# Kernel optimization log

Measured on AMD Instinct MI355X. Metric: run time of the kernel, lower is better.

Reference implementation:

```python
import jax, jax.numpy as jnp
import numpy as np

D = 1  # dilation


def _unfold3x3(x, d):
    # x: [B, C, H, W] -> [B, H*W, 9, C]; matches torch.nn.Unfold(kernel_size=3,
    # dilation=d, padding=d, stride=1) followed by the module's reshapes.
    B, C, H, W = x.shape
    xp = jnp.pad(x, ((0, 0), (0, 0), (d, d), (d, d)))
    pats = [xp[:, :, i * d:i * d + H, j * d:j * d + W] for i in range(3) for j in range(3)]
    p = jnp.stack(pats, axis=0)  # [9, B, C, H, W], kernel positions row-major (center = 4)
    return p.transpose(1, 3, 4, 0, 2).reshape(B, H * W, 9, C)


def _masked_bn(h, m, gamma, beta, eps=1e-5):
    # BatchNorm1d in training mode applied only to rows selected by bool mask m
    # (the torch code gathers rows, BNs them, scatters back into zeros).
    # Stats are the biased mean/var over the selected rows, per channel.
    axes = tuple(range(h.ndim - 1))
    mf = m[..., None].astype(h.dtype)
    n = jnp.maximum(mf.sum(), 1.0)
    mean = (h * mf).sum(axes) / n
    var = (((h - mean) ** 2 * mf)).sum(axes) / n
    return (h - mean) * jax.lax.rsqrt(var + eps) * gamma + beta


def setup_inputs() -> dict:
    key = jax.random.key(0)
    ks = jax.random.split(key, 8)
    B, H, W = 2, 64, 1024
    Cin, Cout, Cm = 64, 64, 4
    s = 0.1
    x = jax.random.normal(ks[0], (B, Cm + Cin, H, W), jnp.float32)
    mask = (jax.random.uniform(ks[1], (B, 1, H, W)) > 0.3).astype(jnp.float32)
    return {
        "x": x,
        "mask": mask,
        "w1": jax.random.normal(ks[2], (8, Cm), jnp.float32) * s,
        "bn1_g": jnp.ones(8, jnp.float32),
        "bn1_b": jnp.zeros(8, jnp.float32),
        "w2": jax.random.normal(ks[3], (1, 8), jnp.float32) * s,
        "b2": jnp.zeros(1, jnp.float32),
        "g1": jax.random.normal(ks[4], (8, Cm), jnp.float32) * s,
        "gbn1_g": jnp.ones(8, jnp.float32),
        "gbn1_b": jnp.zeros(8, jnp.float32),
        "g2": jax.random.normal(ks[5], (8, 8), jnp.float32) * s,
        "gbn2_g": jnp.ones(8, jnp.float32),
        "gbn2_b": jnp.zeros(8, jnp.float32),
        "w_agg": jax.random.normal(ks[6], (Cout, 72 + Cin), jnp.float32) * s,
        "abn_g": jnp.ones(Cout, jnp.float32),
        "abn_b": jnp.zeros(Cout, jnp.float32),
    }


def reference(x, mask, w1, bn1_g, bn1_b, w2, b2, g1, gbn1_g, gbn1_b, g2, gbn2_g, gbn2_b, w_agg, abn_g, abn_b):
    B, C, H, W = x.shape
    xu = _unfold3x3(x, D)                      # [B, HW, 9, C]
    mu = _unfold3x3(mask, D)[..., 0]           # [B, HW, 9]
    msel = mu > 0                              # valid-neighbor mask
    mp0 = msel[:, :, 4]                        # valid-center mask [B, HW]
    pn = xu[..., :4] - xu[:, :, 4:5, :4]       # relative meta coords [B, HW, 9, 4]
    feats = xu[..., 4:]                        # neighbor features [B, HW, 9, Cin]

    # weight branch (dense compute + mask == torch's gather/scatter)
    h = _masked_bn(pn @ w1.T, msel, bn1_g, bn1_b)
    h = jax.nn.relu(h) @ w2.T + b2             # [B, HW, 9, 1]
    wts = jnp.where(msel, h[..., 0], 0.0)      # zeros at invalid neighbors pre-softmax
    wts = jax.nn.softmax(wts, axis=-1)[..., None]

    fagg = (wts * feats).sum(axis=2)           # [B, HW, Cin]

    # geo branch
    g = jax.nn.relu(_masked_bn(pn @ g1.T, msel, gbn1_g, gbn1_b))
    g = jax.nn.relu(_masked_bn(g @ g2.T, msel, gbn2_g, gbn2_b))
    g = jnp.where(msel[..., None], g, 0.0)
    g = (wts * g).reshape(B, H * W, 72)

    # aggregation over valid centers
    out = jnp.concatenate([fagg, g], axis=-1) @ w_agg.T
    out = jax.nn.relu(_masked_bn(out, mp0, abn_g, abn_b))
    out = jnp.where(mp0[..., None], out, 0.0)  # [B, HW, Cout]
    return out.transpose(0, 2, 1).reshape(B, -1, H, W)  # fold with k=1 == reshape
```

## Files before the change

### kernel.cpp

```cpp
#include <hip/hip_runtime.h>

#define HW_ 65536
#define W_ 1024
#define H_ 64
#define B_ 2
#define C_ 68
#define NPIX 131072
#define EPS 1e-5f

typedef __attribute__((ext_vector_type(8))) short short8;
typedef __attribute__((ext_vector_type(4))) float floatx4;

__device__ __forceinline__ unsigned short f2bf(float f) {
  unsigned u = __float_as_uint(f);
  u += 0x7fffu + ((u >> 16) & 1u);
  return (unsigned short)(u >> 16);
}
__device__ __forceinline__ unsigned pack2(float a, float b) {
  return (unsigned)f2bf(a) | ((unsigned)f2bf(b) << 16);
}
__device__ __forceinline__ float wred(float v) {
  v += __shfl_xor(v, 1);  v += __shfl_xor(v, 2);  v += __shfl_xor(v, 4);
  v += __shfl_xor(v, 8);  v += __shfl_xor(v, 16); v += __shfl_xor(v, 32);
  return v;
}
__device__ __forceinline__ int swz_tile(int bid) {
  return (bid & 7) * 64 + (bid >> 3);
}

__global__ __launch_bounds__(256) void k_stats1(
    const float* __restrict__ x, const float* __restrict__ mask,
    const float* __restrict__ w1, const float* __restrict__ g1,
    float* __restrict__ ws) {
  float acc[34];
#pragma unroll
  for (int i = 0; i < 34; i++) acc[i] = 0.f;

  int p = swz_tile(blockIdx.x) * 256 + threadIdx.x;
  {
    int b = p >> 16, s = p & (HW_ - 1);
    int h = s >> 10, w = s & (W_ - 1);
    const float* xb = x + (size_t)b * C_ * HW_;
    const float* mb = mask + (size_t)b * HW_;
    float xc0 = xb[s], xc1 = xb[HW_ + s], xc2 = xb[2 * HW_ + s], xc3 = xb[3 * HW_ + s];
    acc[33] += (mb[s] > 0.f) ? 1.f : 0.f;
#pragma unroll
    for (int k = 0; k < 9; k++) {
      int di = k / 3 - 1, dj = k % 3 - 1;
      int hh = h + di, ww = w + dj;
      bool inb = ((unsigned)hh < (unsigned)H_) && ((unsigned)ww < (unsigned)W_);
      int ns = hh * W_ + ww;
      float mval = inb ? mb[ns] : 0.f;
      if (mval > 0.f) {
        float pn0 = xb[ns] - xc0;
        float pn1 = xb[HW_ + ns] - xc1;
        float pn2 = xb[2 * HW_ + ns] - xc2;
        float pn3 = xb[3 * HW_ + ns] - xc3;
        acc[32] += 1.f;
#pragma unroll
        for (int o = 0; o < 8; o++) {
          float ta = pn0 * w1[o * 4] + pn1 * w1[o * 4 + 1] + pn2 * w1[o * 4 + 2] + pn3 * w1[o * 4 + 3];
          acc[o] += ta; acc[8 + o] += ta * ta;
          float tg = pn0 * g1[o * 4] + pn1 * g1[o * 4 + 1] + pn2 * g1[o * 4 + 2] + pn3 * g1[o * 4 + 3];
          acc[16 + o] += tg; acc[24 + o] += tg * tg;
        }
      }
    }
  }
  __shared__ float red[4][34];
  int lane = threadIdx.x & 63, wave = threadIdx.x >> 6;
#pragma unroll
  for (int i = 0; i < 34; i++) {
    float r = wred(acc[i]);
    if (lane == 0) red[wave][i] = r;
  }
  __syncthreads();
  if (threadIdx.x < 34)
    atomicAdd(&ws[threadIdx.x],
              red[0][threadIdx.x] + red[1][threadIdx.x] + red[2][threadIdx.x] + red[3][threadIdx.x]);
}

__global__ __launch_bounds__(256) void k_stats2(
    const float* __restrict__ x, const float* __restrict__ mask,
    const float* __restrict__ g1, const float* __restrict__ gbn1_g,
    const float* __restrict__ gbn1_b, const float* __restrict__ g2,
    float* __restrict__ ws) {
  __shared__ float sc[8], sh[8];
  if (threadIdx.x < 8) {
    int o = threadIdx.x;
    float n = fmaxf(ws[32], 1.f);
    float mean = ws[16 + o] / n;
    float var = ws[24 + o] / n - mean * mean;
    float s = gbn1_g[o] * rsqrtf(var + EPS);
    sc[o] = s; sh[o] = gbn1_b[o] - mean * s;
  }
  __syncthreads();

  float acc[16];
#pragma unroll
  for (int i = 0; i < 16; i++) acc[i] = 0.f;

  int p = swz_tile(blockIdx.x) * 256 + threadIdx.x;
  {
    int b = p >> 16, s = p & (HW_ - 1);
    int h = s >> 10, w = s & (W_ - 1);
    const float* xb = x + (size_t)b * C_ * HW_;
    const float* mb = mask + (size_t)b * HW_;
    float xc0 = xb[s], xc1 = xb[HW_ + s], xc2 = xb[2 * HW_ + s], xc3 = xb[3 * HW_ + s];
#pragma unroll
    for (int k = 0; k < 9; k++) {
      int di = k / 3 - 1, dj = k % 3 - 1;
      int hh = h + di, ww = w + dj;
      bool inb = ((unsigned)hh < (unsigned)H_) && ((unsigned)ww < (unsigned)W_);
      int ns = hh * W_ + ww;
      float mval = inb ? mb[ns] : 0.f;
      if (mval > 0.f) {
        float pn0 = xb[ns] - xc0;
        float pn1 = xb[HW_ + ns] - xc1;
        float pn2 = xb[2 * HW_ + ns] - xc2;
        float pn3 = xb[3 * HW_ + ns] - xc3;
        float gb[8];
#pragma unroll
        for (int o = 0; o < 8; o++) {
          float tg = pn0 * g1[o * 4] + pn1 * g1[o * 4 + 1] + pn2 * g1[o * 4 + 2] + pn3 * g1[o * 4 + 3];
          gb[o] = fmaxf(sc[o] * tg + sh[o], 0.f);
        }
#pragma unroll
        for (int j = 0; j < 8; j++) {
          float t2 = 0.f;
#pragma unroll
          for (int o = 0; o < 8; o++) t2 += gb[o] * g2[j * 8 + o];
          acc[j] += t2; acc[8 + j] += t2 * t2;
        }
      }
    }
  }
  __shared__ float red[4][16];
  int lane = threadIdx.x & 63, wave = threadIdx.x >> 6;
#pragma unroll
  for (int i = 0; i < 16; i++) {
    float r = wred(acc[i]);
    if (lane == 0) red[wave][i] = r;
  }
  __syncthreads();
  if (threadIdx.x < 16)
    atomicAdd(&ws[40 + threadIdx.x],
              red[0][threadIdx.x] + red[1][threadIdx.x] + red[2][threadIdx.x] + red[3][threadIdx.x]);
}

__global__ __launch_bounds__(256) void k_fused(
    const float* __restrict__ x, const float* __restrict__ mask,
    const float* __restrict__ w1, const float* __restrict__ bn1_g,
    const float* __restrict__ bn1_b, const float* __restrict__ w2,
    const float* __restrict__ b2, const float* __restrict__ g1,
    const float* __restrict__ gbn1_g, const float* __restrict__ gbn1_b,
    const float* __restrict__ g2, const float* __restrict__ gbn2_g,
    const float* __restrict__ gbn2_b, const float* __restrict__ w_agg,
    const float* __restrict__ ws, float* __restrict__ out_pre,
    float* __restrict__ wsum) {
  __shared__ uint4 vecA[17][256];
  __shared__ float sA[8], hA[8], sG1[8], hG1[8], sG2[8], hG2[8];

  if (threadIdx.x < 24) {
    int o = threadIdx.x & 7;
    float n = fmaxf(ws[32], 1.f);
    float sum, sum2, gma, bta;
    if (threadIdx.x < 8)       { sum = ws[o];      sum2 = ws[8 + o];  gma = bn1_g[o];  bta = bn1_b[o]; }
    else if (threadIdx.x < 16) { sum = ws[16 + o]; sum2 = ws[24 + o]; gma = gbn1_g[o]; bta = gbn1_b[o]; }
    else                       { sum = ws[40 + o]; sum2 = ws[48 + o]; gma = gbn2_g[o]; bta = gbn2_b[o]; }
    float mean = sum / n, var = sum2 / n - mean * mean;
    float s = gma * rsqrtf(var + EPS);
    float sft = bta - mean * s;
    if (threadIdx.x < 8)       { sA[o] = s;  hA[o] = sft; }
    else if (threadIdx.x < 16) { sG1[o] = s; hG1[o] = sft; }
    else                       { sG2[o] = s; hG2[o] = sft; }
  }
  __syncthreads();

  int tile = swz_tile(blockIdx.x);
  int p0 = tile * 256;
  int p = p0 + threadIdx.x;
  int b = p >> 16, s = p & (HW_ - 1);
  int h = s >> 10, w = s & (W_ - 1);
  const float* xb = x + (size_t)b * C_ * HW_;
  const float* mb = mask + (size_t)b * HW_;
  float xc0 = xb[s], xc1 = xb[HW_ + s], xc2 = xb[2 * HW_ + s], xc3 = xb[3 * HW_ + s];
  float b2v = b2[0];

  float ev[9]; int nsv[9]; bool inbv[9], mselv[9];
  float mx = -1e30f;
#pragma unroll
  for (int k = 0; k < 9; k++) {
    int di = k / 3 - 1, dj = k % 3 - 1;
    int hh = h + di, ww = w + dj;
    bool inb = ((unsigned)hh < (unsigned)H_) && ((unsigned)ww < (unsigned)W_);
    int ns = hh * W_ + ww;
    inbv[k] = inb; nsv[k] = ns;
    float mval = inb ? mb[ns] : 0.f;
    bool msel = mval > 0.f;
    mselv[k] = msel;
    float wp = 0.f;
    if (msel) {
      float pn0 = xb[ns] - xc0;
      float pn1 = xb[HW_ + ns] - xc1;
      float pn2 = xb[2 * HW_ + ns] - xc2;
      float pn3 = xb[3 * HW_ + ns] - xc3;
      float accw = 0.f;
#pragma unroll
      for (int o = 0; o < 8; o++) {
        float ta = pn0 * w1[o * 4] + pn1 * w1[o * 4 + 1] + pn2 * w1[o * 4 + 2] + pn3 * w1[o * 4 + 3];
        accw += fmaxf(sA[o] * ta + hA[o], 0.f) * w2[o];
      }
      wp = accw + b2v;
    }
    ev[k] = wp;
    mx = fmaxf(mx, wp);
  }
  float den = 0.f;
#pragma unroll
  for (int k = 0; k < 9; k++) { ev[k] = __expf(ev[k] - mx); den += ev[k]; }
  float inv = 1.f / den;

  float fagg[64];
#pragma unroll
  for (int c = 0; c < 64; c++) fagg[c] = 0.f;

#pragma unroll
  for (int k = 0; k < 9; k++) {
    float wt = ev[k] * inv;
    int ns = nsv[k];
    uint4 pk; pk.x = pk.y = pk.z = pk.w = 0u;
    if (mselv[k]) {
      float pn0 = xb[ns] - xc0;
      float pn1 = xb[HW_ + ns] - xc1;
      float pn2 = xb[2 * HW_ + ns] - xc2;
      float pn3 = xb[3 * HW_ + ns] - xc3;
      float gb[8];
#pragma unroll
      for (int o = 0; o < 8; o++) {
        float tg = pn0 * g1[o * 4] + pn1 * g1[o * 4 + 1] + pn2 * g1[o * 4 + 2] + pn3 * g1[o * 4 + 3];
        gb[o] = fmaxf(sG1[o] * tg + hG1[o], 0.f);
      }
      float gv[8];
#pragma unroll
      for (int j = 0; j < 8; j++) {
        float t2 = 0.f;
#pragma unroll
        for (int o = 0; o < 8; o++) t2 += gb[o] * g2[j * 8 + o];
        float gg = fmaxf(sG2[j] * t2 + hG2[j], 0.f);
        gv[j] = wt * gg;
      }
      pk.x = pack2(gv[0], gv[1]); pk.y = pack2(gv[2], gv[3]);
      pk.z = pack2(gv[4], gv[5]); pk.w = pack2(gv[6], gv[7]);
    }
    vecA[8 + k][threadIdx.x] = pk;
    if (inbv[k]) {
      const float* xf = xb + 4 * HW_ + ns;
#pragma unroll
      for (int c = 0; c < 64; c++) fagg[c] += wt * xf[c * HW_];
    }
  }
#pragma unroll
  for (int c = 0; c < 64; c += 8) {
    uint4 pk;
    pk.x = pack2(fagg[c], fagg[c + 1]);     pk.y = pack2(fagg[c + 2], fagg[c + 3]);
    pk.z = pack2(fagg[c + 4], fagg[c + 5]); pk.w = pack2(fagg[c + 6], fagg[c + 7]);
    vecA[c >> 3][threadIdx.x] = pk;
  }
  __syncthreads();

  int lane = threadIdx.x & 63, wave = threadIdx.x >> 6;
  int q = lane >> 4, r = lane & 15;

  short8 Bf[4][5];
#pragma unroll
  for (int nt = 0; nt < 4; nt++) {
    int n = nt * 16 + r;
#pragma unroll
    for (int ks = 0; ks < 5; ks++) {
      int k0 = ks * 32 + q * 8;
      uint4 pk; pk.x = pk.y = pk.z = pk.w = 0u;
      if (k0 < 136) {
        float4 f0 = *reinterpret_cast<const float4*>(w_agg + n * 136 + k0);
        float4 f1 = *reinterpret_cast<const float4*>(w_agg + n * 136 + k0 + 4);
        pk.x = pack2(f0.x, f0.y); pk.y = pack2(f0.z, f0.w);
        pk.z = pack2(f1.x, f1.y); pk.w = pack2(f1.z, f1.w);
      }
      Bf[nt][ks] = *reinterpret_cast<short8*>(&pk);
    }
  }

  floatx4 acc[4][4];
#pragma unroll
  for (int m = 0; m < 4; m++)
#pragma unroll
    for (int nt = 0; nt < 4; nt++) acc[m][nt] = (floatx4){0.f, 0.f, 0.f, 0.f};

#pragma unroll
  for (int m = 0; m < 4; m++) {
    int mt = wave * 4 + m;
    int pix = mt * 16 + r;
    short8 Af[5];
#pragma unroll
    for (int ks = 0; ks < 5; ks++) {
      int chunk = ks * 4 + q;
      if (chunk < 17)
        Af[ks] = *reinterpret_cast<const short8*>(&vecA[chunk][pix]);
      else
        Af[ks] = (short8){0, 0, 0, 0, 0, 0, 0, 0};
    }
#pragma unroll
    for (int nt = 0; nt < 4; nt++)
#pragma unroll
      for (int ks = 0; ks < 5; ks++)
        acc[m][nt] = __builtin_amdgcn_mfma_f32_16x16x32_bf16(Af[ks], Bf[nt][ks], acc[m][nt], 0, 0, 0);
  }

  float aS[4] = {0.f, 0.f, 0.f, 0.f}, aQ[4] = {0.f, 0.f, 0.f, 0.f};
  int s0 = p0 & (HW_ - 1);
#pragma unroll
  for (int m = 0; m < 4; m++) {
    int mt = wave * 4 + m;
    int srow = s0 + mt * 16 + q * 4;
    float4 mv = *reinterpret_cast<const float4*>(mb + srow);
    float m0 = (mv.x > 0.f) ? 1.f : 0.f, m1 = (mv.y > 0.f) ? 1.f : 0.f;
    float m2 = (mv.z > 0.f) ? 1.f : 0.f, m3 = (mv.w > 0.f) ? 1.f : 0.f;
#pragma unroll
    for (int nt = 0; nt < 4; nt++) {
      int ch = nt * 16 + r;
      float4 ov;
      ov.x = acc[m][nt][0]; ov.y = acc[m][nt][1];
      ov.z = acc[m][nt][2]; ov.w = acc[m][nt][3];
      aS[nt] += ov.x * m0 + ov.y * m1 + ov.z * m2 + ov.w * m3;
      aQ[nt] += ov.x * ov.x * m0 + ov.y * ov.y * m1 + ov.z * ov.z * m2 + ov.w * ov.w * m3;
      *reinterpret_cast<float4*>(out_pre + ((size_t)(b * 64 + ch)) * HW_ + srow) = ov;
    }
  }

  __syncthreads();
  float* rS = (float*)&vecA[0][0];
  float* rQ = rS + 256;
#pragma unroll
  for (int nt = 0; nt < 4; nt++) {
    float v1 = aS[nt], v2 = aQ[nt];
    v1 += __shfl_xor(v1, 16); v1 += __shfl_xor(v1, 32);
    v2 += __shfl_xor(v2, 16); v2 += __shfl_xor(v2, 32);
    if (lane < 16) { rS[wave * 64 + nt * 16 + lane] = v1; rQ[wave * 64 + nt * 16 + lane] = v2; }
  }
  __syncthreads();
  if (threadIdx.x < 64) {
    atomicAdd(&wsum[64 + threadIdx.x],
              rS[threadIdx.x] + rS[64 + threadIdx.x] + rS[128 + threadIdx.x] + rS[192 + threadIdx.x]);
    atomicAdd(&wsum[128 + threadIdx.x],
              rQ[threadIdx.x] + rQ[64 + threadIdx.x] + rQ[128 + threadIdx.x] + rQ[192 + threadIdx.x]);
  }
}

__global__ __launch_bounds__(256) void k_final(
    const float* __restrict__ out_pre, const float* __restrict__ mask,
    const float* __restrict__ abn_g, const float* __restrict__ abn_b,
    const float* __restrict__ ws, float* __restrict__ out) {
  __shared__ float sc[64], sh[64];
  if (threadIdx.x < 64) {
    int c = threadIdx.x;
    float n0 = fmaxf(ws[33], 1.f);
    float mean = ws[64 + c] / n0;
    float var = ws[128 + c] / n0 - mean * mean;
    float s = abn_g[c] * rsqrtf(var + EPS);
    sc[c] = s; sh[c] = abn_b[c] - mean * s;
  }
  __syncthreads();
  int i4 = (blockIdx.x * 256 + threadIdx.x) * 4;
  if (i4 >= B_ * 64 * HW_) return;
  int c = (i4 >> 16) & 63;
  int b = i4 >> 22;
  int s = i4 & (HW_ - 1);
  float4 v = *reinterpret_cast<const float4*>(out_pre + i4);
  float4 m = *reinterpret_cast<const float4*>(mask + (size_t)b * HW_ + s);
  float4 o;
  o.x = (m.x > 0.f) ? fmaxf(v.x * sc[c] + sh[c], 0.f) : 0.f;
  o.y = (m.y > 0.f) ? fmaxf(v.y * sc[c] + sh[c], 0.f) : 0.f;
  o.z = (m.z > 0.f) ? fmaxf(v.z * sc[c] + sh[c], 0.f) : 0.f;
  o.w = (m.w > 0.f) ? fmaxf(v.w * sc[c] + sh[c], 0.f) : 0.f;
  *reinterpret_cast<float4*>(out + i4) = o;
}

extern "C" void kernel_launch(void* const* d_in, const int* in_sizes, int n_in,
                              void* d_out, int out_size, void* d_ws, size_t ws_size,
                              hipStream_t stream) {
  const float* x      = (const float*)d_in[0];
  const float* mask   = (const float*)d_in[1];
  const float* w1     = (const float*)d_in[2];
  const float* bn1_g  = (const float*)d_in[3];
  const float* bn1_b  = (const float*)d_in[4];
  const float* w2     = (const float*)d_in[5];
  const float* b2     = (const float*)d_in[6];
  const float* g1     = (const float*)d_in[7];
  const float* gbn1_g = (const float*)d_in[8];
  const float* gbn1_b = (const float*)d_in[9];
  const float* g2     = (const float*)d_in[10];
  const float* gbn2_g = (const float*)d_in[11];
  const float* gbn2_b = (const float*)d_in[12];
  const float* w_agg  = (const float*)d_in[13];
  const float* abn_g  = (const float*)d_in[14];
  const float* abn_b  = (const float*)d_in[15];
  float* out = (float*)d_out;

  size_t need = 1024 + (size_t)NPIX * 64 * 4;
  if (ws_size < need) return;

  float* wsf = (float*)d_ws;
  float* out_pre = (float*)((char*)d_ws + 1024);

  hipMemsetAsync(d_ws, 0, 1024, stream);
  k_stats1<<<512, 256, 0, stream>>>(x, mask, w1, g1, wsf);
  k_stats2<<<512, 256, 0, stream>>>(x, mask, g1, gbn1_g, gbn1_b, g2, wsf);
  k_fused<<<512, 256, 0, stream>>>(x, mask, w1, bn1_g, bn1_b, w2, b2, g1,
                                   gbn1_g, gbn1_b, g2, gbn2_g, gbn2_b, w_agg,
                                   wsf, out_pre, wsf);
  k_final<<<8192, 256, 0, stream>>>(out_pre, mask, abn_g, abn_b, wsf, out);
}
```

Measured before the change: 222.9 us.

## Use moment stats for BN1, split neighbors across waves, store bf16 intermediate

```diff
diff --git a/kernel.cpp b/kernel.cpp
--- a/kernel.cpp
+++ b/kernel.cpp
@@ -3,10 +3,13 @@
 #define HW_ 65536
 #define W_ 1024
 #define H_ 64
-#define B_ 2
 #define C_ 68
 #define NPIX 131072
 #define EPS 1e-5f
+
+#define ST2OFF 256
+#define ATOFF 512
+#define OUTPRE_BYTE 16384
 
 typedef __attribute__((ext_vector_type(8))) short short8;
 typedef __attribute__((ext_vector_type(4))) float floatx4;
@@ -19,65 +22,60 @@
 __device__ __forceinline__ unsigned pack2(float a, float b) {
   return (unsigned)f2bf(a) | ((unsigned)f2bf(b) << 16);
 }
+__device__ __forceinline__ float bf2f(unsigned short u) {
+  return __uint_as_float(((unsigned)u) << 16);
+}
 __device__ __forceinline__ float wred(float v) {
   v += __shfl_xor(v, 1);  v += __shfl_xor(v, 2);  v += __shfl_xor(v, 4);
   v += __shfl_xor(v, 8);  v += __shfl_xor(v, 16); v += __shfl_xor(v, 32);
   return v;
 }
-__device__ __forceinline__ int swz_tile(int bid) {
-  return (bid & 7) * 64 + (bid >> 3);
-}
 
 __global__ __launch_bounds__(256) void k_stats1(
     const float* __restrict__ x, const float* __restrict__ mask,
-    const float* __restrict__ w1, const float* __restrict__ g1,
     float* __restrict__ ws) {
-  float acc[34];
-#pragma unroll
-  for (int i = 0; i < 34; i++) acc[i] = 0.f;
-
-  int p = swz_tile(blockIdx.x) * 256 + threadIdx.x;
-  {
-    int b = p >> 16, s = p & (HW_ - 1);
-    int h = s >> 10, w = s & (W_ - 1);
-    const float* xb = x + (size_t)b * C_ * HW_;
-    const float* mb = mask + (size_t)b * HW_;
-    float xc0 = xb[s], xc1 = xb[HW_ + s], xc2 = xb[2 * HW_ + s], xc3 = xb[3 * HW_ + s];
-    acc[33] += (mb[s] > 0.f) ? 1.f : 0.f;
-#pragma unroll
-    for (int k = 0; k < 9; k++) {
-      int di = k / 3 - 1, dj = k % 3 - 1;
-      int hh = h + di, ww = w + dj;
-      bool inb = ((unsigned)hh < (unsigned)H_) && ((unsigned)ww < (unsigned)W_);
-      int ns = hh * W_ + ww;
-      float mval = inb ? mb[ns] : 0.f;
-      if (mval > 0.f) {
-        float pn0 = xb[ns] - xc0;
-        float pn1 = xb[HW_ + ns] - xc1;
-        float pn2 = xb[2 * HW_ + ns] - xc2;
-        float pn3 = xb[3 * HW_ + ns] - xc3;
-        acc[32] += 1.f;
-#pragma unroll
-        for (int o = 0; o < 8; o++) {
-          float ta = pn0 * w1[o * 4] + pn1 * w1[o * 4 + 1] + pn2 * w1[o * 4 + 2] + pn3 * w1[o * 4 + 3];
-          acc[o] += ta; acc[8 + o] += ta * ta;
-          float tg = pn0 * g1[o * 4] + pn1 * g1[o * 4 + 1] + pn2 * g1[o * 4 + 2] + pn3 * g1[o * 4 + 3];
-          acc[16 + o] += tg; acc[24 + o] += tg * tg;
-        }
-      }
-    }
-  }
-  __shared__ float red[4][34];
-  int lane = threadIdx.x & 63, wave = threadIdx.x >> 6;
-#pragma unroll
-  for (int i = 0; i < 34; i++) {
+  __shared__ float red[4][16];
+  const int tid = threadIdx.x, bid = blockIdx.x;
+  const int lane = tid & 63, wave = tid >> 6;
+  const int seg = (bid & 7) * 256 + (bid >> 3);
+  const int sg = seg * 64 + lane;
+  const int b = sg >> 16, s = sg & (HW_ - 1);
+  const int h = s >> 10, w = s & (W_ - 1);
+  const float* xb = x + (size_t)b * C_ * HW_;
+  const float* mb = mask + (size_t)b * HW_;
+
+  float acc[16];
+#pragma unroll
+  for (int i = 0; i < 16; i++) acc[i] = 0.f;
+  float xc0 = xb[s], xc1 = xb[HW_ + s], xc2 = xb[2 * HW_ + s], xc3 = xb[3 * HW_ + s];
+  if (wave == 0) acc[15] = (mb[s] > 0.f) ? 1.f : 0.f;
+
+  for (int k = wave; k < 9; k += 4) {
+    int di = k / 3 - 1, dj = k % 3 - 1;
+    int hh = h + di, ww = w + dj;
+    bool inb = ((unsigned)hh < (unsigned)H_) && ((unsigned)ww < (unsigned)W_);
+    int ns = inb ? hh * W_ + ww : s;
+    float mk = (inb && mb[ns] > 0.f) ? 1.f : 0.f;
+    float p0 = xb[ns] - xc0;
+    float p1 = xb[HW_ + ns] - xc1;
+    float p2 = xb[2 * HW_ + ns] - xc2;
+    float p3 = xb[3 * HW_ + ns] - xc3;
+    float q0 = mk * p0, q1 = mk * p1, q2 = mk * p2, q3 = mk * p3;
+    acc[0] += q0; acc[1] += q1; acc[2] += q2; acc[3] += q3;
+    acc[4] += q0 * p0; acc[5] += q0 * p1; acc[6] += q0 * p2; acc[7] += q0 * p3;
+    acc[8] += q1 * p1; acc[9] += q1 * p2; acc[10] += q1 * p3;
+    acc[11] += q2 * p2; acc[12] += q2 * p3;
+    acc[13] += q3 * p3;
+    acc[14] += mk;
+  }
+#pragma unroll
+  for (int i = 0; i < 16; i++) {
     float r = wred(acc[i]);
     if (lane == 0) red[wave][i] = r;
   }
   __syncthreads();
-  if (threadIdx.x < 34)
-    atomicAdd(&ws[threadIdx.x],
-              red[0][threadIdx.x] + red[1][threadIdx.x] + red[2][threadIdx.x] + red[3][threadIdx.x]);
+  if (tid < 16)
+    atomicAdd(&ws[tid * 16], red[0][tid] + red[1][tid] + red[2][tid] + red[3][tid]);
 }
 
 __global__ __launch_bounds__(256) void k_stats2(
@@ -85,67 +83,71 @@
     const float* __restrict__ g1, const float* __restrict__ gbn1_g,
     const float* __restrict__ gbn1_b, const float* __restrict__ g2,
     float* __restrict__ ws) {
-  __shared__ float sc[8], sh[8];
-  if (threadIdx.x < 8) {
-    int o = threadIdx.x;
-    float n = fmaxf(ws[32], 1.f);
-    float mean = ws[16 + o] / n;
-    float var = ws[24 + o] / n - mean * mean;
-    float s = gbn1_g[o] * rsqrtf(var + EPS);
-    sc[o] = s; sh[o] = gbn1_b[o] - mean * s;
-  }
-  __syncthreads();
+  __shared__ float scl[16];
+  __shared__ float red[4][16];
+  const int tid = threadIdx.x, bid = blockIdx.x;
+  const int lane = tid & 63, wave = tid >> 6;
+
+  if (tid < 8) {
+    int o = tid;
+    float n = fmaxf(ws[224], 1.f);
+    const float* wv = g1 + o * 4;
+    float w0 = wv[0], w1v = wv[1], w2v = wv[2], w3v = wv[3];
+    float sum = w0 * ws[0] + w1v * ws[16] + w2v * ws[32] + w3v * ws[48];
+    float quad = w0 * (w0 * ws[64] + 2.f * (w1v * ws[80] + w2v * ws[96] + w3v * ws[112]))
+               + w1v * (w1v * ws[128] + 2.f * (w2v * ws[144] + w3v * ws[160]))
+               + w2v * (w2v * ws[176] + 2.f * w3v * ws[192])
+               + w3v * w3v * ws[208];
+    float mean = sum / n, var = quad / n - mean * mean;
+    float sv = gbn1_g[o] * rsqrtf(var + EPS);
+    scl[o] = sv; scl[8 + o] = gbn1_b[o] - mean * sv;
+  }
+  __syncthreads();
+
+  const int seg = (bid & 7) * 256 + (bid >> 3);
+  const int sg = seg * 64 + lane;
+  const int b = sg >> 16, s = sg & (HW_ - 1);
+  const int h = s >> 10, w = s & (W_ - 1);
+  const float* xb = x + (size_t)b * C_ * HW_;
+  const float* mb = mask + (size_t)b * HW_;
 
   float acc[16];
 #pragma unroll
   for (int i = 0; i < 16; i++) acc[i] = 0.f;
-
-  int p = swz_tile(blockIdx.x) * 256 + threadIdx.x;
-  {
-    int b = p >> 16, s = p & (HW_ - 1);
-    int h = s >> 10, w = s & (W_ - 1);
-    const float* xb = x + (size_t)b * C_ * HW_;
-    const float* mb = mask + (size_t)b * HW_;
-    float xc0 = xb[s], xc1 = xb[HW_ + s], xc2 = xb[2 * HW_ + s], xc3 = xb[3 * HW_ + s];
-#pragma unroll
-    for (int k = 0; k < 9; k++) {
-      int di = k / 3 - 1, dj = k % 3 - 1;
-      int hh = h + di, ww = w + dj;
-      bool inb = ((unsigned)hh < (unsigned)H_) && ((unsigned)ww < (unsigned)W_);
-      int ns = hh * W_ + ww;
-      float mval = inb ? mb[ns] : 0.f;
-      if (mval > 0.f) {
-        float pn0 = xb[ns] - xc0;
-        float pn1 = xb[HW_ + ns] - xc1;
-        float pn2 = xb[2 * HW_ + ns] - xc2;
-        float pn3 = xb[3 * HW_ + ns] - xc3;
-        float gb[8];
-#pragma unroll
-        for (int o = 0; o < 8; o++) {
-          float tg = pn0 * g1[o * 4] + pn1 * g1[o * 4 + 1] + pn2 * g1[o * 4 + 2] + pn3 * g1[o * 4 + 3];
-          gb[o] = fmaxf(sc[o] * tg + sh[o], 0.f);
-        }
-#pragma unroll
-        for (int j = 0; j < 8; j++) {
-          float t2 = 0.f;
-#pragma unroll
-          for (int o = 0; o < 8; o++) t2 += gb[o] * g2[j * 8 + o];
-          acc[j] += t2; acc[8 + j] += t2 * t2;
-        }
-      }
-    }
-  }
-  __shared__ float red[4][16];
-  int lane = threadIdx.x & 63, wave = threadIdx.x >> 6;
+  float xc0 = xb[s], xc1 = xb[HW_ + s], xc2 = xb[2 * HW_ + s], xc3 = xb[3 * HW_ + s];
+
+  for (int k = wave; k < 9; k += 4) {
+    int di = k / 3 - 1, dj = k % 3 - 1;
+    int hh = h + di, ww = w + dj;
+    bool inb = ((unsigned)hh < (unsigned)H_) && ((unsigned)ww < (unsigned)W_);
+    int ns = inb ? hh * W_ + ww : s;
+    float mk = (inb && mb[ns] > 0.f) ? 1.f : 0.f;
+    float pn0 = xb[ns] - xc0;
+    float pn1 = xb[HW_ + ns] - xc1;
+    float pn2 = xb[2 * HW_ + ns] - xc2;
+    float pn3 = xb[3 * HW_ + ns] - xc3;
+    float gb[8];
+#pragma unroll
+    for (int o = 0; o < 8; o++) {
+      float tg = pn0 * g1[o * 4] + pn1 * g1[o * 4 + 1] + pn2 * g1[o * 4 + 2] + pn3 * g1[o * 4 + 3];
+      gb[o] = fmaxf(scl[o] * tg + scl[8 + o], 0.f);
+    }
+#pragma unroll
+    for (int j = 0; j < 8; j++) {
+      float t2 = 0.f;
+#pragma unroll
+      for (int o = 0; o < 8; o++) t2 += gb[o] * g2[j * 8 + o];
+      acc[j] += mk * t2; acc[8 + j] += mk * t2 * t2;
+    }
+  }
 #pragma unroll
   for (int i = 0; i < 16; i++) {
     float r = wred(acc[i]);
     if (lane == 0) red[wave][i] = r;
   }
   __syncthreads();
-  if (threadIdx.x < 16)
-    atomicAdd(&ws[40 + threadIdx.x],
-              red[0][threadIdx.x] + red[1][threadIdx.x] + red[2][threadIdx.x] + red[3][threadIdx.x]);
+  if (tid < 16)
+    atomicAdd(&ws[ST2OFF + tid * 16], red[0][tid] + red[1][tid] + red[2][tid] + red[3][tid]);
 }
 
 __global__ __launch_bounds__(256) void k_fused(
@@ -156,30 +158,41 @@
     const float* __restrict__ gbn1_g, const float* __restrict__ gbn1_b,
     const float* __restrict__ g2, const float* __restrict__ gbn2_g,
     const float* __restrict__ gbn2_b, const float* __restrict__ w_agg,
-    const float* __restrict__ ws, float* __restrict__ out_pre,
-    float* __restrict__ wsum) {
+    float* __restrict__ ws) {
   __shared__ uint4 vecA[17][256];
   __shared__ float sA[8], hA[8], sG1[8], hG1[8], sG2[8], hG2[8];
-
-  if (threadIdx.x < 24) {
-    int o = threadIdx.x & 7;
-    float n = fmaxf(ws[32], 1.f);
-    float sum, sum2, gma, bta;
-    if (threadIdx.x < 8)       { sum = ws[o];      sum2 = ws[8 + o];  gma = bn1_g[o];  bta = bn1_b[o]; }
-    else if (threadIdx.x < 16) { sum = ws[16 + o]; sum2 = ws[24 + o]; gma = gbn1_g[o]; bta = gbn1_b[o]; }
-    else                       { sum = ws[40 + o]; sum2 = ws[48 + o]; gma = gbn2_g[o]; bta = gbn2_b[o]; }
-    float mean = sum / n, var = sum2 / n - mean * mean;
-    float s = gma * rsqrtf(var + EPS);
-    float sft = bta - mean * s;
-    if (threadIdx.x < 8)       { sA[o] = s;  hA[o] = sft; }
-    else if (threadIdx.x < 16) { sG1[o] = s; hG1[o] = sft; }
-    else                       { sG2[o] = s; hG2[o] = sft; }
-  }
-  __syncthreads();
-
-  int tile = swz_tile(blockIdx.x);
+  const int tid = threadIdx.x;
+
+  if (tid < 24) {
+    int o = tid & 7;
+    float n = fmaxf(ws[224], 1.f);
+    float sv, sft;
+    if (tid < 16) {
+      const float* wv = (tid < 8) ? (w1 + o * 4) : (g1 + o * 4);
+      float w0 = wv[0], w1v = wv[1], w2v = wv[2], w3v = wv[3];
+      float sum = w0 * ws[0] + w1v * ws[16] + w2v * ws[32] + w3v * ws[48];
+      float quad = w0 * (w0 * ws[64] + 2.f * (w1v * ws[80] + w2v * ws[96] + w3v * ws[112]))
+                 + w1v * (w1v * ws[128] + 2.f * (w2v * ws[144] + w3v * ws[160]))
+                 + w2v * (w2v * ws[176] + 2.f * w3v * ws[192])
+                 + w3v * w3v * ws[208];
+      float gma = (tid < 8) ? bn1_g[o] : gbn1_g[o];
+      float bta = (tid < 8) ? bn1_b[o] : gbn1_b[o];
+      float mean = sum / n, var = quad / n - mean * mean;
+      sv = gma * rsqrtf(var + EPS); sft = bta - mean * sv;
+    } else {
+      float sum = ws[ST2OFF + o * 16], sum2 = ws[ST2OFF + (8 + o) * 16];
+      float mean = sum / n, var = sum2 / n - mean * mean;
+      sv = gbn2_g[o] * rsqrtf(var + EPS); sft = gbn2_b[o] - mean * sv;
+    }
+    if (tid < 8)       { sA[o] = sv;  hA[o] = sft; }
+    else if (tid < 16) { sG1[o] = sv; hG1[o] = sft; }
+    else               { sG2[o] = sv; hG2[o] = sft; }
+  }
+  __syncthreads();
+
+  int tile = (blockIdx.x & 7) * 64 + (blockIdx.x >> 3);
   int p0 = tile * 256;
-  int p = p0 + threadIdx.x;
+  int p = p0 + tid;
   int b = p >> 16, s = p & (HW_ - 1);
   int h = s >> 10, w = s & (W_ - 1);
   const float* xb = x + (size_t)b * C_ * HW_;
@@ -187,32 +200,30 @@
   float xc0 = xb[s], xc1 = xb[HW_ + s], xc2 = xb[2 * HW_ + s], xc3 = xb[3 * HW_ + s];
   float b2v = b2[0];
 
-  float ev[9]; int nsv[9]; bool inbv[9], mselv[9];
+  float ev[9], mkv[9], ibv[9]; int nsv[9];
   float mx = -1e30f;
 #pragma unroll
   for (int k = 0; k < 9; k++) {
     int di = k / 3 - 1, dj = k % 3 - 1;
     int hh = h + di, ww = w + dj;
     bool inb = ((unsigned)hh < (unsigned)H_) && ((unsigned)ww < (unsigned)W_);
-    int ns = hh * W_ + ww;
-    inbv[k] = inb; nsv[k] = ns;
-    float mval = inb ? mb[ns] : 0.f;
-    bool msel = mval > 0.f;
-    mselv[k] = msel;
-    float wp = 0.f;
-    if (msel) {
-      float pn0 = xb[ns] - xc0;
-      float pn1 = xb[HW_ + ns] - xc1;
-      float pn2 = xb[2 * HW_ + ns] - xc2;
-      float pn3 = xb[3 * HW_ + ns] - xc3;
-      float accw = 0.f;
-#pragma unroll
-      for (int o = 0; o < 8; o++) {
-        float ta = pn0 * w1[o * 4] + pn1 * w1[o * 4 + 1] + pn2 * w1[o * 4 + 2] + pn3 * w1[o * 4 + 3];
-        accw += fmaxf(sA[o] * ta + hA[o], 0.f) * w2[o];
-      }
-      wp = accw + b2v;
-    }
+    int ns = inb ? hh * W_ + ww : s;
+    nsv[k] = ns;
+    ibv[k] = inb ? 1.f : 0.f;
+    float mval = mb[ns];
+    float mk = (inb && mval > 0.f) ? 1.f : 0.f;
+    mkv[k] = mk;
+    float pn0 = xb[ns] - xc0;
+    float pn1 = xb[HW_ + ns] - xc1;
+    float pn2 = xb[2 * HW_ + ns] - xc2;
+    float pn3 = xb[3 * HW_ + ns] - xc3;
+    float accw = 0.f;
+#pragma unroll
+    for (int o = 0; o < 8; o++) {
+      float ta = pn0 * w1[o * 4] + pn1 * w1[o * 4 + 1] + pn2 * w1[o * 4 + 2] + pn3 * w1[o * 4 + 3];
+      accw += fmaxf(sA[o] * ta + hA[o], 0.f) * w2[o];
+    }
+    float wp = mk * (accw + b2v);
     ev[k] = wp;
     mx = fmaxf(mx, wp);
   }
@@ -229,47 +240,44 @@
   for (int k = 0; k < 9; k++) {
     float wt = ev[k] * inv;
     int ns = nsv[k];
-    uint4 pk; pk.x = pk.y = pk.z = pk.w = 0u;
-    if (mselv[k]) {
-      float pn0 = xb[ns] - xc0;
-      float pn1 = xb[HW_ + ns] - xc1;
-      float pn2 = xb[2 * HW_ + ns] - xc2;
-      float pn3 = xb[3 * HW_ + ns] - xc3;
-      float gb[8];
-#pragma unroll
-      for (int o = 0; o < 8; o++) {
-        float tg = pn0 * g1[o * 4] + pn1 * g1[o * 4 + 1] + pn2 * g1[o * 4 + 2] + pn3 * g1[o * 4 + 3];
-        gb[o] = fmaxf(sG1[o] * tg + hG1[o], 0.f);
-      }
-      float gv[8];
-#pragma unroll
-      for (int j = 0; j < 8; j++) {
-        float t2 = 0.f;
-#pragma unroll
-        for (int o = 0; o < 8; o++) t2 += gb[o] * g2[j * 8 + o];
-        float gg = fmaxf(sG2[j] * t2 + hG2[j], 0.f);
-        gv[j] = wt * gg;
-      }
-      pk.x = pack2(gv[0], gv[1]); pk.y = pack2(gv[2], gv[3]);
-      pk.z = pack2(gv[4], gv[5]); pk.w = pack2(gv[6], gv[7]);
-    }
-    vecA[8 + k][threadIdx.x] = pk;
-    if (inbv[k]) {
-      const float* xf = xb + 4 * HW_ + ns;
-#pragma unroll
-      for (int c = 0; c < 64; c++) fagg[c] += wt * xf[c * HW_];
-    }
+    float wg = wt * mkv[k];
+    float pn0 = xb[ns] - xc0;
+    float pn1 = xb[HW_ + ns] - xc1;
+    float pn2 = xb[2 * HW_ + ns] - xc2;
+    float pn3 = xb[3 * HW_ + ns] - xc3;
+    float gb[8];
+#pragma unroll
+    for (int o = 0; o < 8; o++) {
+      float tg = pn0 * g1[o * 4] + pn1 * g1[o * 4 + 1] + pn2 * g1[o * 4 + 2] + pn3 * g1[o * 4 + 3];
+      gb[o] = fmaxf(sG1[o] * tg + hG1[o], 0.f);
+    }
+    float gv[8];
+#pragma unroll
+    for (int j = 0; j < 8; j++) {
+      float t2 = 0.f;
+#pragma unroll
+      for (int o = 0; o < 8; o++) t2 += gb[o] * g2[j * 8 + o];
+      gv[j] = wg * fmaxf(sG2[j] * t2 + hG2[j], 0.f);
+    }
+    uint4 pk;
+    pk.x = pack2(gv[0], gv[1]); pk.y = pack2(gv[2], gv[3]);
+    pk.z = pack2(gv[4], gv[5]); pk.w = pack2(gv[6], gv[7]);
+    vecA[8 + k][tid] = pk;
+    float wf = wt * ibv[k];
+    const float* xf = xb + 4 * HW_ + ns;
+#pragma unroll
+    for (int c = 0; c < 64; c++) fagg[c] += wf * xf[c * HW_];
   }
 #pragma unroll
   for (int c = 0; c < 64; c += 8) {
     uint4 pk;
     pk.x = pack2(fagg[c], fagg[c + 1]);     pk.y = pack2(fagg[c + 2], fagg[c + 3]);
     pk.z = pack2(fagg[c + 4], fagg[c + 5]); pk.w = pack2(fagg[c + 6], fagg[c + 7]);
-    vecA[c >> 3][threadIdx.x] = pk;
-  }
-  __syncthreads();
-
-  int lane = threadIdx.x & 63, wave = threadIdx.x >> 6;
+    vecA[c >> 3][tid] = pk;
+  }
+  __syncthreads();
+
+  int lane = tid & 63, wave = tid >> 6;
   int q = lane >> 4, r = lane & 15;
 
   short8 Bf[4][5];
@@ -298,14 +306,13 @@
 
 #pragma unroll
   for (int m = 0; m < 4; m++) {
-    int mt = wave * 4 + m;
-    int pix = mt * 16 + r;
+    int pix = (wave * 4 + m) * 16 + r;
     short8 Af[5];
 #pragma unroll
     for (int ks = 0; ks < 5; ks++) {
-      int chunk = ks * 4 + q;
-      if (chunk < 17)
-        Af[ks] = *reinterpret_cast<const short8*>(&vecA[chunk][pix]);
+      int ch = ks * 4 + q;
+      if (ch < 17)
+        Af[ks] = *reinterpret_cast<const short8*>(&vecA[ch][pix]);
       else
         Af[ks] = (short8){0, 0, 0, 0, 0, 0, 0, 0};
     }
@@ -317,23 +324,23 @@
   }
 
   float aS[4] = {0.f, 0.f, 0.f, 0.f}, aQ[4] = {0.f, 0.f, 0.f, 0.f};
+  unsigned short* out_pre = (unsigned short*)((char*)ws + OUTPRE_BYTE);
   int s0 = p0 & (HW_ - 1);
 #pragma unroll
   for (int m = 0; m < 4; m++) {
-    int mt = wave * 4 + m;
-    int srow = s0 + mt * 16 + q * 4;
+    int srow = s0 + (wave * 4 + m) * 16 + q * 4;
     float4 mv = *reinterpret_cast<const float4*>(mb + srow);
     float m0 = (mv.x > 0.f) ? 1.f : 0.f, m1 = (mv.y > 0.f) ? 1.f : 0.f;
     float m2 = (mv.z > 0.f) ? 1.f : 0.f, m3 = (mv.w > 0.f) ? 1.f : 0.f;
 #pragma unroll
     for (int nt = 0; nt < 4; nt++) {
       int ch = nt * 16 + r;
-      float4 ov;
-      ov.x = acc[m][nt][0]; ov.y = acc[m][nt][1];
-      ov.z = acc[m][nt][2]; ov.w = acc[m][nt][3];
-      aS[nt] += ov.x * m0 + ov.y * m1 + ov.z * m2 + ov.w * m3;
-      aQ[nt] += ov.x * ov.x * m0 + ov.y * ov.y * m1 + ov.z * ov.z * m2 + ov.w * ov.w * m3;
-      *reinterpret_cast<float4*>(out_pre + ((size_t)(b * 64 + ch)) * HW_ + srow) = ov;
+      float o0 = acc[m][nt][0], o1 = acc[m][nt][1], o2 = acc[m][nt][2], o3 = acc[m][nt][3];
+      aS[nt] += o0 * m0 + o1 * m1 + o2 * m2 + o3 * m3;
+      aQ[nt] += o0 * o0 * m0 + o1 * o1 * m1 + o2 * o2 * m2 + o3 * o3 * m3;
+      uint2 pk;
+      pk.x = pack2(o0, o1); pk.y = pack2(o2, o3);
+      *reinterpret_cast<uint2*>(out_pre + (size_t)(b * 64 + ch) * HW_ + srow) = pk;
     }
   }
 
@@ -348,41 +355,48 @@
     if (lane < 16) { rS[wave * 64 + nt * 16 + lane] = v1; rQ[wave * 64 + nt * 16 + lane] = v2; }
   }
   __syncthreads();
-  if (threadIdx.x < 64) {
-    atomicAdd(&wsum[64 + threadIdx.x],
-              rS[threadIdx.x] + rS[64 + threadIdx.x] + rS[128 + threadIdx.x] + rS[192 + threadIdx.x]);
-    atomicAdd(&wsum[128 + threadIdx.x],
-              rQ[threadIdx.x] + rQ[64 + threadIdx.x] + rQ[128 + threadIdx.x] + rQ[192 + threadIdx.x]);
+  if (tid < 64) {
+    atomicAdd(&ws[ATOFF + tid * 16],
+              rS[tid] + rS[64 + tid] + rS[128 + tid] + rS[192 + tid]);
+    atomicAdd(&ws[ATOFF + (64 + tid) * 16],
+              rQ[tid] + rQ[64 + tid] + rQ[128 + tid] + rQ[192 + tid]);
   }
 }
 
 __global__ __launch_bounds__(256) void k_final(
-    const float* __restrict__ out_pre, const float* __restrict__ mask,
-    const float* __restrict__ abn_g, const float* __restrict__ abn_b,
-    const float* __restrict__ ws, float* __restrict__ out) {
+    const float* __restrict__ mask, const float* __restrict__ abn_g,
+    const float* __restrict__ abn_b, const float* __restrict__ ws,
+    float* __restrict__ out) {
   __shared__ float sc[64], sh[64];
   if (threadIdx.x < 64) {
     int c = threadIdx.x;
-    float n0 = fmaxf(ws[33], 1.f);
-    float mean = ws[64 + c] / n0;
-    float var = ws[128 + c] / n0 - mean * mean;
+    float n0 = fmaxf(ws[240], 1.f);
+    float mean = ws[ATOFF + c * 16] / n0;
+    float var = ws[ATOFF + (64 + c) * 16] / n0 - mean * mean;
     float s = abn_g[c] * rsqrtf(var + EPS);
     sc[c] = s; sh[c] = abn_b[c] - mean * s;
   }
   __syncthreads();
-  int i4 = (blockIdx.x * 256 + threadIdx.x) * 4;
-  if (i4 >= B_ * 64 * HW_) return;
-  int c = (i4 >> 16) & 63;
-  int b = i4 >> 22;
-  int s = i4 & (HW_ - 1);
-  float4 v = *reinterpret_cast<const float4*>(out_pre + i4);
-  float4 m = *reinterpret_cast<const float4*>(mask + (size_t)b * HW_ + s);
-  float4 o;
-  o.x = (m.x > 0.f) ? fmaxf(v.x * sc[c] + sh[c], 0.f) : 0.f;
-  o.y = (m.y > 0.f) ? fmaxf(v.y * sc[c] + sh[c], 0.f) : 0.f;
-  o.z = (m.z > 0.f) ? fmaxf(v.z * sc[c] + sh[c], 0.f) : 0.f;
-  o.w = (m.w > 0.f) ? fmaxf(v.w * sc[c] + sh[c], 0.f) : 0.f;
-  *reinterpret_cast<float4*>(out + i4) = o;
+  const unsigned short* out_pre = (const unsigned short*)((const char*)ws + OUTPRE_BYTE);
+  int i8 = (blockIdx.x * 256 + threadIdx.x) * 8;
+  int c = (i8 >> 16) & 63;
+  int b = i8 >> 22;
+  int s = i8 & (HW_ - 1);
+  uint4 v = *reinterpret_cast<const uint4*>(out_pre + i8);
+  float4 ma = *reinterpret_cast<const float4*>(mask + (size_t)b * HW_ + s);
+  float4 mb4 = *reinterpret_cast<const float4*>(mask + (size_t)b * HW_ + s + 4);
+  float scc = sc[c], shc = sh[c];
+  float4 o0, o1;
+  o0.x = (ma.x > 0.f) ? fmaxf(bf2f((unsigned short)(v.x & 0xffff)) * scc + shc, 0.f) : 0.f;
+  o0.y = (ma.y > 0.f) ? fmaxf(bf2f((unsigned short)(v.x >> 16)) * scc + shc, 0.f) : 0.f;
+  o0.z = (ma.z > 0.f) ? fmaxf(bf2f((unsigned short)(v.y & 0xffff)) * scc + shc, 0.f) : 0.f;
+  o0.w = (ma.w > 0.f) ? fmaxf(bf2f((unsigned short)(v.y >> 16)) * scc + shc, 0.f) : 0.f;
+  o1.x = (mb4.x > 0.f) ? fmaxf(bf2f((unsigned short)(v.z & 0xffff)) * scc + shc, 0.f) : 0.f;
+  o1.y = (mb4.y > 0.f) ? fmaxf(bf2f((unsigned short)(v.z >> 16)) * scc + shc, 0.f) : 0.f;
+  o1.z = (mb4.z > 0.f) ? fmaxf(bf2f((unsigned short)(v.w & 0xffff)) * scc + shc, 0.f) : 0.f;
+  o1.w = (mb4.w > 0.f) ? fmaxf(bf2f((unsigned short)(v.w >> 16)) * scc + shc, 0.f) : 0.f;
+  *reinterpret_cast<float4*>(out + i8) = o0;
+  *reinterpret_cast<float4*>(out + i8 + 4) = o1;
 }
 
 extern "C" void kernel_launch(void* const* d_in, const int* in_sizes, int n_in,
@@ -406,17 +420,14 @@
   const float* abn_b  = (const float*)d_in[15];
   float* out = (float*)d_out;
 
-  size_t need = 1024 + (size_t)NPIX * 64 * 4;
+  size_t need = (size_t)OUTPRE_BYTE + (size_t)NPIX * 64 * 2;
   if (ws_size < need) return;
 
   float* wsf = (float*)d_ws;
-  float* out_pre = (float*)((char*)d_ws + 1024);
-
-  hipMemsetAsync(d_ws, 0, 1024, stream);
-  k_stats1<<<512, 256, 0, stream>>>(x, mask, w1, g1, wsf);
-  k_stats2<<<512, 256, 0, stream>>>(x, mask, g1, gbn1_g, gbn1_b, g2, wsf);
+  hipMemsetAsync(d_ws, 0, OUTPRE_BYTE, stream);
+  k_stats1<<<2048, 256, 0, stream>>>(x, mask, wsf);
+  k_stats2<<<2048, 256, 0, stream>>>(x, mask, g1, gbn1_g, gbn1_b, g2, wsf);
   k_fused<<<512, 256, 0, stream>>>(x, mask, w1, bn1_g, bn1_b, w2, b2, g1,
-                                   gbn1_g, gbn1_b, g2, gbn2_g, gbn2_b, w_agg,
-                                   wsf, out_pre, wsf);
-  k_final<<<8192, 256, 0, stream>>>(out_pre, mask, abn_g, abn_b, wsf, out);
-}
+                                   gbn1_g, gbn1_b, g2, gbn2_g, gbn2_b, w_agg, wsf);
+  k_final<<<4096, 256, 0, stream>>>(mask, abn_g, abn_b, wsf, out);
+}
```

After: 307.4 us. 37.9% more time.
